# Performance work log

Hardware: AMD Instinct MI355X
Metric: run time of the kernel (lower is better)

## Reference

```python
import jax, jax.numpy as jnp
import numpy as np

B, S, E, H, SN, LMAX = 128, 512, 768, 16, 100, 5
DH = E // H  # 48

def setup_inputs() -> dict:
    key = jax.random.key(0)
    ks = jax.random.split(key, 10)
    idx = jax.random.randint(ks[0], (B, LMAX), 0, S)
    lengths = jax.random.randint(ks[1], (B,), 1, LMAX + 1)
    valid = jnp.arange(LMAX)[None, :] < lengths[:, None]
    locations = jnp.where(valid, idx, -1)
    return {
        "last_hidden_state": jax.random.normal(ks[2], (B, S, E), jnp.float32),
        "sense_emb": jax.random.normal(ks[3], (B, SN, E), jnp.float32),
        "locations": locations,
        "in_proj_weight": jax.random.normal(ks[4], (3 * E, E), jnp.float32) * 0.02,
        "in_proj_bias": jax.random.normal(ks[5], (3 * E,), jnp.float32) * 0.02,
        "out_proj_weight": jax.random.normal(ks[6], (E, E), jnp.float32) * 0.02,
        "out_proj_bias": jax.random.normal(ks[7], (E,), jnp.float32) * 0.02,
        "linear_weight": jax.random.normal(ks[8], (SN, E), jnp.float32) * 0.02,
        "linear_bias": jax.random.normal(ks[9], (SN,), jnp.float32) * 0.02,
    }

def reference(last_hidden_state, sense_emb, locations, in_proj_weight, in_proj_bias,
              out_proj_weight, out_proj_bias, linear_weight, linear_bias):
    # Ragged gather + mean over the valid (non -1) token locations per row.
    mask = (locations != -1)                                   # [B, LMAX]
    safe = jnp.where(mask, locations, 0)                       # [B, LMAX]
    gathered = jnp.take_along_axis(last_hidden_state, safe[..., None], axis=1)  # [B,LMAX,E]
    cnt = mask.sum(axis=1, keepdims=True).astype(last_hidden_state.dtype)
    pun = (gathered * mask[..., None]).sum(axis=1) / cnt       # [B, E]

    # qkv: prepend pun-word embedding to the sense embeddings -> [B, SN+1, E]
    qkv = jnp.concatenate([pun[:, None, :], sense_emb], axis=1)

    # nn.MultiheadAttention with batch_first=False: axis0 = seq (L=B), axis1 = batch (N=SN+1).
    proj = qkv @ in_proj_weight.T + in_proj_bias               # [L, N, 3E]
    q, k, v = jnp.split(proj, 3, axis=-1)
    L, N = qkv.shape[0], qkv.shape[1]
    q = q.reshape(L, N, H, DH) * (DH ** -0.5)
    k = k.reshape(L, N, H, DH)
    v = v.reshape(L, N, H, DH)
    scores = jnp.einsum('lnhd,mnhd->nhlm', q, k)               # [N,H,L,L]
    attn = jax.nn.softmax(scores, axis=-1)
    ctx = jnp.einsum('nhlm,mnhd->lnhd', attn, v).reshape(L, N, E)
    attn_out = ctx @ out_proj_weight.T + out_proj_bias         # [L, N, E]

    res = attn_out[:, 0, :]                                    # [B, E] (batch slot 0)
    res = res @ linear_weight.T + linear_bias                  # [B, SN]
    return res
```

## Files before the change

### kernel.cpp

```cpp
#include <hip/hip_runtime.h>

#define SEQ 512
#define EMB 768
#define K3E 2304
#define DHD 48

__global__ __launch_bounds__(256) void k1_gemm1(
    const float* __restrict__ lhs, const int* __restrict__ loc,
    const float* __restrict__ Bw, const float* __restrict__ bias,
    float* __restrict__ C)
{
  __shared__ float lds[7168];
  const int t  = threadIdx.x;
  const int w  = t >> 6, l = t & 63;
  const int bm = blockIdx.y * 16, bn = blockIdx.x * 32;
  const int tx = l & 7, ty = l >> 3;
  const int gm = l & 15, gq = l >> 4;
  const int bl = l & 31, bh = l >> 5;
  const int kbase = w * 192;
  const int AW = w * 1792, BW = AW + 640;

  int locs[5]; int cnt = 0;
#pragma unroll
  for (int j = 0; j < 5; j++) {
    int v = loc[(bm + gm) * 5 + j];
    locs[j] = v; if (v >= 0) cnt++;
  }
  const float ginv = 1.0f / (float)cnt;
  const float* lrow = lhs + (size_t)(bm + gm) * SEQ * EMB;
  const float* brow = Bw + (size_t)(bn + bl) * EMB;

  float4 aF, bF0, bF1;

#define K1_LOAD(s) {                                                         \
    int k0 = kbase + (s) * 16;                                               \
    float sx=0.f, sy=0.f, sz=0.f, sw=0.f;                                    \
    _Pragma("unroll")                                                        \
    for (int j = 0; j < 5; j++) {                                            \
      int v = locs[j] >= 0 ? locs[j] : 0;                                    \
      float4 wv = *(const float4*)&lrow[(size_t)v * EMB + k0 + gq * 4];      \
      if (locs[j] >= 0) { sx+=wv.x; sy+=wv.y; sz+=wv.z; sw+=wv.w; }          \
    }                                                                        \
    aF = make_float4(sx*ginv, sy*ginv, sz*ginv, sw*ginv);                    \
    bF0 = *(const float4*)&brow[k0 + bh * 8 + 0];                            \
    bF1 = *(const float4*)&brow[k0 + bh * 8 + 4]; }

#define K1_WRITE(b) {                                                        \
    int Ab = AW + (b) * 320;                                                 \
    lds[Ab + (gq*4+0)*20 + gm] = aF.x;                                       \
    lds[Ab + (gq*4+1)*20 + gm] = aF.y;                                       \
    lds[Ab + (gq*4+2)*20 + gm] = aF.z;                                       \
    lds[Ab + (gq*4+3)*20 + gm] = aF.w;                                       \
    int Bb = BW + (b) * 576;                                                 \
    lds[Bb + (bh*8+0)*36 + bl] = bF0.x; lds[Bb + (bh*8+1)*36 + bl] = bF0.y;  \
    lds[Bb + (bh*8+2)*36 + bl] = bF0.z; lds[Bb + (bh*8+3)*36 + bl] = bF0.w;  \
    lds[Bb + (bh*8+4)*36 + bl] = bF1.x; lds[Bb + (bh*8+5)*36 + bl] = bF1.y;  \
    lds[Bb + (bh*8+6)*36 + bl] = bF1.z; lds[Bb + (bh*8+7)*36 + bl] = bF1.w; }

  float acc[2][4] = {};
  K1_LOAD(0); K1_WRITE(0);
  for (int s = 0; s < 12; s++) {
    int b = s & 1;
    if (s < 11) K1_LOAD(s + 1);
    int Ab = AW + b * 320, Bb = BW + b * 576;
#pragma unroll
    for (int kk = 0; kk < 16; kk++) {
      float2 a  = *(float2*)&lds[Ab + kk * 20 + ty * 2];
      float4 bb = *(float4*)&lds[Bb + kk * 36 + tx * 4];
      acc[0][0] += a.x*bb.x; acc[0][1] += a.x*bb.y; acc[0][2] += a.x*bb.z; acc[0][3] += a.x*bb.w;
      acc[1][0] += a.y*bb.x; acc[1][1] += a.y*bb.y; acc[1][2] += a.y*bb.z; acc[1][3] += a.y*bb.w;
    }
    if (s < 11) K1_WRITE(b ^ 1);
  }
#undef K1_LOAD
#undef K1_WRITE

#pragma unroll
  for (int i = 0; i < 2; i++)
    *(float4*)&lds[AW + (ty*2 + i) * 32 + tx * 4] =
        make_float4(acc[i][0], acc[i][1], acc[i][2], acc[i][3]);
  __syncthreads();
  int o = t * 2;
  int m = o >> 5, n = o & 31;
  float2 s0 = *(float2*)&lds[0*1792 + o];
  float2 s1 = *(float2*)&lds[1*1792 + o];
  float2 s2 = *(float2*)&lds[2*1792 + o];
  float2 s3 = *(float2*)&lds[3*1792 + o];
  float2 bb2 = *(const float2*)&bias[bn + n];
  float2 r = make_float2(s0.x+s1.x+s2.x+s3.x+bb2.x, s0.y+s1.y+s2.y+s3.y+bb2.y);
  *(float2*)&C[(size_t)(bm + m) * K3E + bn + n] = r;
}

__global__ __launch_bounds__(256) void k2_attn_wcomb(
    const float* __restrict__ proj, float* __restrict__ ctx,
    const float* __restrict__ wlin, const float* __restrict__ wout,
    float* __restrict__ wcomb)
{
  __shared__ float lds[13312];
  const int t = threadIdx.x;

  if (blockIdx.x < 128) {
    float* ks = lds;
    float* vs = lds + 6656;
    int h  = blockIdx.x >> 3;
    int l0 = (blockIdx.x & 7) * 16;

    for (int i = t; i < 128 * 12; i += 256) {
      int m  = i / 12;
      int dd = (i - m * 12) * 4;
      float4 kv = *(const float4*)&proj[(size_t)m * K3E + EMB     + h * DHD + dd];
      float4 vv = *(const float4*)&proj[(size_t)m * K3E + 2 * EMB + h * DHD + dd];
      *(float4*)&ks[m * 52 + dd] = kv;
      *(float4*)&vs[m * 52 + dd] = vv;
    }

    int l  = t >> 4;
    int g  = t & 15;
    int lg = l0 + l;
    const float scale = 0.14433756729740643f;
    float q[48];
#pragma unroll
    for (int jj = 0; jj < 12; jj++) {
      float4 qv = *(const float4*)&proj[(size_t)lg * K3E + h * DHD + jj * 4];
      q[jj*4+0] = qv.x * scale; q[jj*4+1] = qv.y * scale;
      q[jj*4+2] = qv.z * scale; q[jj*4+3] = qv.w * scale;
    }
    __syncthreads();

    float sv[8];
    float smax = -1e30f;
#pragma unroll
    for (int jm = 0; jm < 8; jm++) {
      int m = g + jm * 16;
      float s = 0.0f;
#pragma unroll
      for (int dq = 0; dq < 12; dq++) {
        float4 kv = *(const float4*)&ks[m * 52 + dq * 4];
        s += q[dq*4+0]*kv.x + q[dq*4+1]*kv.y + q[dq*4+2]*kv.z + q[dq*4+3]*kv.w;
      }
      sv[jm] = s;
      smax = fmaxf(smax, s);
    }
#pragma unroll
    for (int off = 1; off < 16; off <<= 1) smax = fmaxf(smax, __shfl_xor(smax, off));
    float ssum = 0.0f;
#pragma unroll
    for (int jm = 0; jm < 8; jm++) { float e = __expf(sv[jm] - smax); sv[jm] = e; ssum += e; }
#pragma unroll
    for (int off = 1; off < 16; off <<= 1) ssum += __shfl_xor(ssum, off);
    float inv = 1.0f / ssum;
#pragma unroll
    for (int jm = 0; jm < 8; jm++) sv[jm] *= inv;

    float acc[48] = {};
#pragma unroll
    for (int jm = 0; jm < 8; jm++) {
      int m = g + jm * 16;
      float p = sv[jm];
#pragma unroll
      for (int dq = 0; dq < 12; dq++) {
        float4 vv = *(const float4*)&vs[m * 52 + dq * 4];
        acc[dq*4+0] += p*vv.x; acc[dq*4+1] += p*vv.y;
        acc[dq*4+2] += p*vv.z; acc[dq*4+3] += p*vv.w;
      }
    }

    {
      float buf[24];
      if (g & 8) {
#pragma unroll
        for (int d = 0; d < 24; d++) buf[d] = acc[d];
      } else {
#pragma unroll
        for (int d = 0; d < 24; d++) buf[d] = acc[d + 24];
      }
#pragma unroll
      for (int d = 0; d < 24; d++) buf[d] = __shfl_xor(buf[d], 8);
      if (g & 8) {
#pragma unroll
        for (int d = 0; d < 24; d++) acc[d] = acc[d + 24] + buf[d];
      } else {
#pragma unroll
        for (int d = 0; d < 24; d++) acc[d] = acc[d] + buf[d];
      }
    }
    {
      float buf[12];
      if (g & 4) {
#pragma unroll
        for (int d = 0; d < 12; d++) buf[d] = acc[d];
      } else {
#pragma unroll
        for (int d = 0; d < 12; d++) buf[d] = acc[d + 12];
      }
#pragma unroll
      for (int d = 0; d < 12; d++) buf[d] = __shfl_xor(buf[d], 4);
      if (g & 4) {
#pragma unroll
        for (int d = 0; d < 12; d++) acc[d] = acc[d + 12] + buf[d];
      } else {
#pragma unroll
        for (int d = 0; d < 12; d++) acc[d] = acc[d] + buf[d];
      }
    }
    {
      float buf[6];
      if (g & 2) {
#pragma unroll
        for (int d = 0; d < 6; d++) buf[d] = acc[d];
      } else {
#pragma unroll
        for (int d = 0; d < 6; d++) buf[d] = acc[d + 6];
      }
#pragma unroll
      for (int d = 0; d < 6; d++) buf[d] = __shfl_xor(buf[d], 2);
      if (g & 2) {
#pragma unroll
        for (int d = 0; d < 6; d++) acc[d] = acc[d + 6] + buf[d];
      } else {
#pragma unroll
        for (int d = 0; d < 6; d++) acc[d] = acc[d] + buf[d];
      }
    }
    {
      float buf[3];
      if (g & 1) {
#pragma unroll
        for (int d = 0; d < 3; d++) buf[d] = acc[d];
      } else {
#pragma unroll
        for (int d = 0; d < 3; d++) buf[d] = acc[d + 3];
      }
#pragma unroll
      for (int d = 0; d < 3; d++) buf[d] = __shfl_xor(buf[d], 1);
      if (g & 1) {
#pragma unroll
        for (int d = 0; d < 3; d++) acc[d] = acc[d + 3] + buf[d];
      } else {
#pragma unroll
        for (int d = 0; d < 3; d++) acc[d] = acc[d] + buf[d];
      }
    }
#pragma unroll
    for (int j = 0; j < 3; j++) {
      ctx[(size_t)lg * EMB + h * DHD + g * 3 + j] = acc[j];
    }
  } else {
    const int c  = blockIdx.x - 128;
    const int bm = (c / 24) * 16;
    const int bn = (c % 24) * 32;
    const int w  = t >> 6, l = t & 63;
    const int tx = l & 7, ty = l >> 3;
    const int am = l & 15, aq = l >> 4;
    const int wi = l >> 2;
    const int j4 = (l & 3) * 8;
    const int kbase = w * 192;
    const int AW = w * 1792, BW = AW + 640;

    int arow_i = bm + am; if (arow_i > 99) arow_i = 99;
    const float* arow = wlin + (size_t)arow_i * EMB;

    float4 aF, bF0, bF1;

#define W_LOAD(s) {                                                          \
    int k0 = kbase + (s) * 16;                                               \
    aF  = *(const float4*)&arow[k0 + aq * 4];                                \
    const float* wr = wout + (size_t)(k0 + wi) * EMB + bn + j4;              \
    bF0 = *(const float4*)&wr[0];                                            \
    bF1 = *(const float4*)&wr[4]; }

#define W_WRITE(b) {                                                         \
    int Ab = AW + (b) * 320;                                                 \
    lds[Ab + (aq*4+0)*20 + am] = aF.x;                                       \
    lds[Ab + (aq*4+1)*20 + am] = aF.y;                                       \
    lds[Ab + (aq*4+2)*20 + am] = aF.z;                                       \
    lds[Ab + (aq*4+3)*20 + am] = aF.w;                                       \
    int Bb = BW + (b) * 576;                                                 \
    *(float4*)&lds[Bb + wi*36 + j4]     = bF0;                               \
    *(float4*)&lds[Bb + wi*36 + j4 + 4] = bF1; }

    float acc[2][4] = {};
    W_LOAD(0); W_WRITE(0);
    for (int s = 0; s < 12; s++) {
      int b = s & 1;
      if (s < 11) W_LOAD(s + 1);
      int Ab = AW + b * 320, Bb = BW + b * 576;
#pragma unroll
      for (int kk = 0; kk < 16; kk++) {
        float2 a  = *(float2*)&lds[Ab + kk * 20 + ty * 2];
        float4 bb = *(float4*)&lds[Bb + kk * 36 + tx * 4];
        acc[0][0] += a.x*bb.x; acc[0][1] += a.x*bb.y; acc[0][2] += a.x*bb.z; acc[0][3] += a.x*bb.w;
        acc[1][0] += a.y*bb.x; acc[1][1] += a.y*bb.y; acc[1][2] += a.y*bb.z; acc[1][3] += a.y*bb.w;
      }
      if (s < 11) W_WRITE(b ^ 1);
    }
#undef W_LOAD
#undef W_WRITE

#pragma unroll
    for (int i = 0; i < 2; i++)
      *(float4*)&lds[AW + (ty*2 + i) * 32 + tx * 4] =
          make_float4(acc[i][0], acc[i][1], acc[i][2], acc[i][3]);
    __syncthreads();
    int o = t * 2;
    int m = o >> 5, n = o & 31;
    if (bm + m < 100) {
      float2 s0 = *(float2*)&lds[0*1792 + o];
      float2 s1 = *(float2*)&lds[1*1792 + o];
      float2 s2 = *(float2*)&lds[2*1792 + o];
      float2 s3 = *(float2*)&lds[3*1792 + o];
      float2 r = make_float2(s0.x+s1.x+s2.x+s3.x, s0.y+s1.y+s2.y+s3.y);
      *(float2*)&wcomb[(size_t)(bm + m) * EMB + bn + n] = r;
    }
  }
}

__global__ __launch_bounds__(256) void k3_final(
    const float* __restrict__ A, const float* __restrict__ Bw,
    const float* __restrict__ wlin, const float* __restrict__ bout,
    const float* __restrict__ blin, float* __restrict__ C)
{
  __shared__ float lds[7200];
  const int t  = threadIdx.x;
  const int w  = t >> 6, l = t & 63;
  const int bm = blockIdx.y * 16, bn = blockIdx.x * 32;
  const int tx = l & 7, ty = l >> 3;
  const int am = l & 15, aq = l >> 4;
  const int bl = l & 31, bh = l >> 5;
  const int kbase = w * 192;
  const int AW = w * 1792, BW = AW + 640;

  {
    int col = bn + (t >> 3);
    int ks  = (t & 7) * 96;
    float p = 0.f;
    if (col < 100) {
      const float* wr = wlin + (size_t)col * EMB + ks;
#pragma unroll
      for (int j = 0; j < 24; j++) {
        float4 wv = *(const float4*)&wr[j * 4];
        float4 bv = *(const float4*)&bout[ks + j * 4];
        p += wv.x*bv.x + wv.y*bv.y + wv.z*bv.z + wv.w*bv.w;
      }
    }
    p += __shfl_xor(p, 1); p += __shfl_xor(p, 2); p += __shfl_xor(p, 4);
    if ((t & 7) == 0) lds[7168 + (t >> 3)] = p + (col < 100 ? blin[col] : 0.f);
  }

  const float* arow = A + (size_t)(bm + am) * EMB;
  int brow_i = bn + bl; if (brow_i > 99) brow_i = 99;
  const float* brow = Bw + (size_t)brow_i * EMB;

  float4 aF, bF0, bF1;

#define F_LOAD(s) {                                                          \
    int k0 = kbase + (s) * 16;                                               \
    aF  = *(const float4*)&arow[k0 + aq * 4];                                \
    bF0 = *(const float4*)&brow[k0 + bh * 8 + 0];                            \
    bF1 = *(const float4*)&brow[k0 + bh * 8 + 4]; }

#define F_WRITE(b) {                                                         \
    int Ab = AW + (b) * 320;                                                 \
    lds[Ab + (aq*4+0)*20 + am] = aF.x;                                       \
    lds[Ab + (aq*4+1)*20 + am] = aF.y;                                       \
    lds[Ab + (aq*4+2)*20 + am] = aF.z;                                       \
    lds[Ab + (aq*4+3)*20 + am] = aF.w;                                       \
    int Bb = BW + (b) * 576;                                                 \
    lds[Bb + (bh*8+0)*36 + bl] = bF0.x; lds[Bb + (bh*8+1)*36 + bl] = bF0.y;  \
    lds[Bb + (bh*8+2)*36 + bl] = bF0.z; lds[Bb + (bh*8+3)*36 + bl] = bF0.w;  \
    lds[Bb + (bh*8+4)*36 + bl] = bF1.x; lds[Bb + (bh*8+5)*36 + bl] = bF1.y;  \
    lds[Bb + (bh*8+6)*36 + bl] = bF1.z; lds[Bb + (bh*8+7)*36 + bl] = bF1.w; }

  float acc[2][4] = {};
  F_LOAD(0); F_WRITE(0);
  for (int s = 0; s < 12; s++) {
    int b = s & 1;
    if (s < 11) F_LOAD(s + 1);
    int Ab = AW + b * 320, Bb = BW + b * 576;
#pragma unroll
    for (int kk = 0; kk < 16; kk++) {
      float2 a  = *(float2*)&lds[Ab + kk * 20 + ty * 2];
      float4 bb = *(float4*)&lds[Bb + kk * 36 + tx * 4];
      acc[0][0] += a.x*bb.x; acc[0][1] += a.x*bb.y; acc[0][2] += a.x*bb.z; acc[0][3] += a.x*bb.w;
      acc[1][0] += a.y*bb.x; acc[1][1] += a.y*bb.y; acc[1][2] += a.y*bb.z; acc[1][3] += a.y*bb.w;
    }
    if (s < 11) F_WRITE(b ^ 1);
  }
#undef F_LOAD
#undef F_WRITE

#pragma unroll
  for (int i = 0; i < 2; i++)
    *(float4*)&lds[AW + (ty*2 + i) * 32 + tx * 4] =
        make_float4(acc[i][0], acc[i][1], acc[i][2], acc[i][3]);
  __syncthreads();
  int o = t * 2;
  int m = o >> 5, n = o & 31;
#pragma unroll
  for (int j = 0; j < 2; j++) {
    int col = bn + n + j;
    if (col < 100) {
      float v = lds[0*1792 + o + j] + lds[1*1792 + o + j] +
                lds[2*1792 + o + j] + lds[3*1792 + o + j] + lds[7168 + n + j];
      C[(size_t)(bm + m) * 100 + col] = v;
    }
  }
}

extern "C" void kernel_launch(void* const* d_in, const int* in_sizes, int n_in,
                              void* d_out, int out_size, void* d_ws, size_t ws_size,
                              hipStream_t stream) {
  const float* lhs   = (const float*)d_in[0];
  const int*   loc   = (const int*)  d_in[2];
  const float* w_in  = (const float*)d_in[3];
  const float* b_in  = (const float*)d_in[4];
  const float* w_out = (const float*)d_in[5];
  const float* b_out = (const float*)d_in[6];
  const float* w_lin = (const float*)d_in[7];
  const float* b_lin = (const float*)d_in[8];
  float* out = (float*)d_out;

  char* ws = (char*)d_ws;
  float* proj  = (float*)(ws);
  float* ctx   = (float*)(ws + 1179648);
  float* wcomb = (float*)(ws + 1179648 + 393216);

  k1_gemm1<<<dim3(72, 8), 256, 0, stream>>>(lhs, loc, w_in, b_in, proj);
  k2_attn_wcomb<<<296, 256, 0, stream>>>(proj, ctx, w_lin, w_out, wcomb);
  k3_final<<<dim3(4, 8), 256, 0, stream>>>(ctx, wcomb, w_lin, b_out, b_lin, out);
}
```

Baseline: 51.70 us.

## Double split-K waves to 8 per block and hoist pun gathers ahead of GEMM loop

The first projection GEMM and the final GEMM now use 512-thread blocks with 8 waves, each covering 96 of the K dimension instead of 192. Partial sums are reduced across the 8 waves in LDS. In the projection kernel, all the pun-word gather-and-mean loads for a thread's K slice are issued upfront into registers before the GEMM loop, so those scattered loads overlap instead of sitting on the critical path each stage. The changes aim to expose more parallelism and memory-level concurrency, at the cost of more registers, twice the LDS per block, and a larger cross-wave reduction.

```diff
diff --git a/kernel.cpp b/kernel.cpp
--- a/kernel.cpp
+++ b/kernel.cpp
@@ -5,90 +5,102 @@
 #define K3E 2304
 #define DHD 48
 
-__global__ __launch_bounds__(256) void k1_gemm1(
+__global__ __launch_bounds__(512, 4) void k1_proj(
     const float* __restrict__ lhs, const int* __restrict__ loc,
     const float* __restrict__ Bw, const float* __restrict__ bias,
     float* __restrict__ C)
 {
-  __shared__ float lds[7168];
-  const int t  = threadIdx.x;
-  const int w  = t >> 6, l = t & 63;
-  const int bm = blockIdx.y * 16, bn = blockIdx.x * 32;
+  __shared__ float lds[14336];
+  const int t = threadIdx.x;
+  const int w = t >> 6, l = t & 63;
   const int tx = l & 7, ty = l >> 3;
   const int gm = l & 15, gq = l >> 4;
   const int bl = l & 31, bh = l >> 5;
-  const int kbase = w * 192;
+  const int kbase = w * 96;
   const int AW = w * 1792, BW = AW + 640;
-
-  int locs[5]; int cnt = 0;
-#pragma unroll
-  for (int j = 0; j < 5; j++) {
-    int v = loc[(bm + gm) * 5 + j];
-    locs[j] = v; if (v >= 0) cnt++;
-  }
+  const int bm = ((int)blockIdx.x / 72) * 16, bn = ((int)blockIdx.x % 72) * 32;
+
+  int locs[5];
+#pragma unroll
+  for (int j = 0; j < 5; j++) locs[j] = loc[(bm + gm) * 5 + j];
+  int cnt = 0;
+#pragma unroll
+  for (int j = 0; j < 5; j++) if (locs[j] >= 0) cnt++;
   const float ginv = 1.0f / (float)cnt;
   const float* lrow = lhs + (size_t)(bm + gm) * SEQ * EMB;
+
+  float4 pA[6];
+#pragma unroll
+  for (int s = 0; s < 6; s++) {
+    int k0 = kbase + s * 16 + gq * 4;
+    float sx = 0.f, sy = 0.f, sz = 0.f, sw = 0.f;
+#pragma unroll
+    for (int j = 0; j < 5; j++) {
+      int v = locs[j] >= 0 ? locs[j] : 0;
+      float4 wv = *(const float4*)&lrow[(size_t)v * EMB + k0];
+      if (locs[j] >= 0) { sx += wv.x; sy += wv.y; sz += wv.z; sw += wv.w; }
+    }
+    pA[s] = make_float4(sx * ginv, sy * ginv, sz * ginv, sw * ginv);
+  }
+
   const float* brow = Bw + (size_t)(bn + bl) * EMB;
-
-  float4 aF, bF0, bF1;
-
-#define K1_LOAD(s) {                                                         \
+  float4 bF0, bF1;
+  float acc[2][4] = {};
+
+#define B_LOAD(s) {                                                          \
     int k0 = kbase + (s) * 16;                                               \
-    float sx=0.f, sy=0.f, sz=0.f, sw=0.f;                                    \
-    _Pragma("unroll")                                                        \
-    for (int j = 0; j < 5; j++) {                                            \
-      int v = locs[j] >= 0 ? locs[j] : 0;                                    \
-      float4 wv = *(const float4*)&lrow[(size_t)v * EMB + k0 + gq * 4];      \
-      if (locs[j] >= 0) { sx+=wv.x; sy+=wv.y; sz+=wv.z; sw+=wv.w; }          \
-    }                                                                        \
-    aF = make_float4(sx*ginv, sy*ginv, sz*ginv, sw*ginv);                    \
     bF0 = *(const float4*)&brow[k0 + bh * 8 + 0];                            \
     bF1 = *(const float4*)&brow[k0 + bh * 8 + 4]; }
 
-#define K1_WRITE(b) {                                                        \
+#define A_WRITE(b, av) {                                                     \
     int Ab = AW + (b) * 320;                                                 \
-    lds[Ab + (gq*4+0)*20 + gm] = aF.x;                                       \
-    lds[Ab + (gq*4+1)*20 + gm] = aF.y;                                       \
-    lds[Ab + (gq*4+2)*20 + gm] = aF.z;                                       \
-    lds[Ab + (gq*4+3)*20 + gm] = aF.w;                                       \
+    lds[Ab + (gq*4+0)*20 + gm] = (av).x;                                     \
+    lds[Ab + (gq*4+1)*20 + gm] = (av).y;                                     \
+    lds[Ab + (gq*4+2)*20 + gm] = (av).z;                                     \
+    lds[Ab + (gq*4+3)*20 + gm] = (av).w; }
+
+#define B_WRITE(b) {                                                         \
     int Bb = BW + (b) * 576;                                                 \
     lds[Bb + (bh*8+0)*36 + bl] = bF0.x; lds[Bb + (bh*8+1)*36 + bl] = bF0.y;  \
     lds[Bb + (bh*8+2)*36 + bl] = bF0.z; lds[Bb + (bh*8+3)*36 + bl] = bF0.w;  \
     lds[Bb + (bh*8+4)*36 + bl] = bF1.x; lds[Bb + (bh*8+5)*36 + bl] = bF1.y;  \
     lds[Bb + (bh*8+6)*36 + bl] = bF1.z; lds[Bb + (bh*8+7)*36 + bl] = bF1.w; }
 
-  float acc[2][4] = {};
-  K1_LOAD(0); K1_WRITE(0);
-  for (int s = 0; s < 12; s++) {
+#define INNER(b) {                                                           \
+    int Ab = AW + (b) * 320, Bb = BW + (b) * 576;                            \
+    _Pragma("unroll")                                                        \
+    for (int kk = 0; kk < 16; kk++) {                                        \
+      float2 a  = *(float2*)&lds[Ab + kk * 20 + ty * 2];                     \
+      float4 bb = *(float4*)&lds[Bb + kk * 36 + tx * 4];                     \
+      acc[0][0] += a.x*bb.x; acc[0][1] += a.x*bb.y;                          \
+      acc[0][2] += a.x*bb.z; acc[0][3] += a.x*bb.w;                          \
+      acc[1][0] += a.y*bb.x; acc[1][1] += a.y*bb.y;                          \
+      acc[1][2] += a.y*bb.z; acc[1][3] += a.y*bb.w;                          \
+    } }
+
+  B_LOAD(0); A_WRITE(0, pA[0]); B_WRITE(0);
+#pragma unroll
+  for (int s = 0; s < 6; s++) {
     int b = s & 1;
-    if (s < 11) K1_LOAD(s + 1);
-    int Ab = AW + b * 320, Bb = BW + b * 576;
-#pragma unroll
-    for (int kk = 0; kk < 16; kk++) {
-      float2 a  = *(float2*)&lds[Ab + kk * 20 + ty * 2];
-      float4 bb = *(float4*)&lds[Bb + kk * 36 + tx * 4];
-      acc[0][0] += a.x*bb.x; acc[0][1] += a.x*bb.y; acc[0][2] += a.x*bb.z; acc[0][3] += a.x*bb.w;
-      acc[1][0] += a.y*bb.x; acc[1][1] += a.y*bb.y; acc[1][2] += a.y*bb.z; acc[1][3] += a.y*bb.w;
-    }
-    if (s < 11) K1_WRITE(b ^ 1);
-  }
-#undef K1_LOAD
-#undef K1_WRITE
+    if (s < 5) B_LOAD(s + 1);
+    INNER(b);
+    if (s < 5) { A_WRITE(b ^ 1, pA[s + 1]); B_WRITE(b ^ 1); }
+  }
+#undef B_LOAD
+#undef A_WRITE
+#undef B_WRITE
+#undef INNER
 
 #pragma unroll
   for (int i = 0; i < 2; i++)
     *(float4*)&lds[AW + (ty*2 + i) * 32 + tx * 4] =
         make_float4(acc[i][0], acc[i][1], acc[i][2], acc[i][3]);
   __syncthreads();
-  int o = t * 2;
-  int m = o >> 5, n = o & 31;
-  float2 s0 = *(float2*)&lds[0*1792 + o];
-  float2 s1 = *(float2*)&lds[1*1792 + o];
-  float2 s2 = *(float2*)&lds[2*1792 + o];
-  float2 s3 = *(float2*)&lds[3*1792 + o];
-  float2 bb2 = *(const float2*)&bias[bn + n];
-  float2 r = make_float2(s0.x+s1.x+s2.x+s3.x+bb2.x, s0.y+s1.y+s2.y+s3.y+bb2.y);
-  *(float2*)&C[(size_t)(bm + m) * K3E + bn + n] = r;
+  int m = t >> 5, n = t & 31;
+  float v = lds[0*1792 + t] + lds[1*1792 + t] + lds[2*1792 + t] + lds[3*1792 + t]
+          + lds[4*1792 + t] + lds[5*1792 + t] + lds[6*1792 + t] + lds[7*1792 + t]
+          + bias[bn + n];
+  C[(size_t)(bm + m) * K3E + bn + n] = v;
 }
 
 __global__ __launch_bounds__(256) void k2_attn_wcomb(
@@ -247,8 +259,7 @@
     }
   } else {
     const int c  = blockIdx.x - 128;
-    const int bm = (c / 24) * 16;
-    const int bn = (c % 24) * 32;
+    const int bm = (c / 24) * 16, bn = (c % 24) * 32;
     const int w  = t >> 6, l = t & 63;
     const int tx = l & 7, ty = l >> 3;
     const int am = l & 15, aq = l >> 4;
@@ -315,22 +326,22 @@
   }
 }
 
-__global__ __launch_bounds__(256) void k3_final(
+__global__ __launch_bounds__(512, 4) void k3_final(
     const float* __restrict__ A, const float* __restrict__ Bw,
     const float* __restrict__ wlin, const float* __restrict__ bout,
     const float* __restrict__ blin, float* __restrict__ C)
 {
-  __shared__ float lds[7200];
-  const int t  = threadIdx.x;
-  const int w  = t >> 6, l = t & 63;
+  __shared__ float lds[14368];
+  const int t = threadIdx.x;
+  const int w = t >> 6, l = t & 63;
   const int bm = blockIdx.y * 16, bn = blockIdx.x * 32;
   const int tx = l & 7, ty = l >> 3;
-  const int am = l & 15, aq = l >> 4;
+  const int gm = l & 15, gq = l >> 4;
   const int bl = l & 31, bh = l >> 5;
-  const int kbase = w * 192;
+  const int kbase = w * 96;
   const int AW = w * 1792, BW = AW + 640;
 
-  {
+  if (t < 256) {
     int col = bn + (t >> 3);
     int ks  = (t & 7) * 96;
     float p = 0.f;
@@ -344,10 +355,10 @@
       }
     }
     p += __shfl_xor(p, 1); p += __shfl_xor(p, 2); p += __shfl_xor(p, 4);
-    if ((t & 7) == 0) lds[7168 + (t >> 3)] = p + (col < 100 ? blin[col] : 0.f);
-  }
-
-  const float* arow = A + (size_t)(bm + am) * EMB;
+    if ((t & 7) == 0) lds[14336 + (t >> 3)] = p + (col < 100 ? blin[col] : 0.f);
+  }
+
+  const float* arow = A + (size_t)(bm + gm) * EMB;
   int brow_i = bn + bl; if (brow_i > 99) brow_i = 99;
   const float* brow = Bw + (size_t)brow_i * EMB;
 
@@ -355,16 +366,16 @@
 
 #define F_LOAD(s) {                                                          \
     int k0 = kbase + (s) * 16;                                               \
-    aF  = *(const float4*)&arow[k0 + aq * 4];                                \
+    aF  = *(const float4*)&arow[k0 + gq * 4];                                \
     bF0 = *(const float4*)&brow[k0 + bh * 8 + 0];                            \
     bF1 = *(const float4*)&brow[k0 + bh * 8 + 4]; }
 
 #define F_WRITE(b) {                                                         \
     int Ab = AW + (b) * 320;                                                 \
-    lds[Ab + (aq*4+0)*20 + am] = aF.x;                                       \
-    lds[Ab + (aq*4+1)*20 + am] = aF.y;                                       \
-    lds[Ab + (aq*4+2)*20 + am] = aF.z;                                       \
-    lds[Ab + (aq*4+3)*20 + am] = aF.w;                                       \
+    lds[Ab + (gq*4+0)*20 + gm] = aF.x;                                       \
+    lds[Ab + (gq*4+1)*20 + gm] = aF.y;                                       \
+    lds[Ab + (gq*4+2)*20 + gm] = aF.z;                                       \
+    lds[Ab + (gq*4+3)*20 + gm] = aF.w;                                       \
     int Bb = BW + (b) * 576;                                                 \
     lds[Bb + (bh*8+0)*36 + bl] = bF0.x; lds[Bb + (bh*8+1)*36 + bl] = bF0.y;  \
     lds[Bb + (bh*8+2)*36 + bl] = bF0.z; lds[Bb + (bh*8+3)*36 + bl] = bF0.w;  \
@@ -373,9 +384,9 @@
 
   float acc[2][4] = {};
   F_LOAD(0); F_WRITE(0);
-  for (int s = 0; s < 12; s++) {
+  for (int s = 0; s < 6; s++) {
     int b = s & 1;
-    if (s < 11) F_LOAD(s + 1);
+    if (s < 5) F_LOAD(s + 1);
     int Ab = AW + b * 320, Bb = BW + b * 576;
 #pragma unroll
     for (int kk = 0; kk < 16; kk++) {
@@ -384,7 +395,7 @@
       acc[0][0] += a.x*bb.x; acc[0][1] += a.x*bb.y; acc[0][2] += a.x*bb.z; acc[0][3] += a.x*bb.w;
       acc[1][0] += a.y*bb.x; acc[1][1] += a.y*bb.y; acc[1][2] += a.y*bb.z; acc[1][3] += a.y*bb.w;
     }
-    if (s < 11) F_WRITE(b ^ 1);
+    if (s < 5) F_WRITE(b ^ 1);
   }
 #undef F_LOAD
 #undef F_WRITE
@@ -394,16 +405,13 @@
     *(float4*)&lds[AW + (ty*2 + i) * 32 + tx * 4] =
         make_float4(acc[i][0], acc[i][1], acc[i][2], acc[i][3]);
   __syncthreads();
-  int o = t * 2;
-  int m = o >> 5, n = o & 31;
-#pragma unroll
-  for (int j = 0; j < 2; j++) {
-    int col = bn + n + j;
-    if (col < 100) {
-      float v = lds[0*1792 + o + j] + lds[1*1792 + o + j] +
-                lds[2*1792 + o + j] + lds[3*1792 + o + j] + lds[7168 + n + j];
-      C[(size_t)(bm + m) * 100 + col] = v;
-    }
+  int m = t >> 5, n = t & 31;
+  int col = bn + n;
+  if (col < 100) {
+    float v = lds[0*1792 + t] + lds[1*1792 + t] + lds[2*1792 + t] + lds[3*1792 + t]
+            + lds[4*1792 + t] + lds[5*1792 + t] + lds[6*1792 + t] + lds[7*1792 + t]
+            + lds[14336 + n];
+    C[(size_t)(bm + m) * 100 + col] = v;
   }
 }
 
@@ -423,9 +431,9 @@
   char* ws = (char*)d_ws;
   float* proj  = (float*)(ws);
   float* ctx   = (float*)(ws + 1179648);
-  float* wcomb = (float*)(ws + 1179648 + 393216);
-
-  k1_gemm1<<<dim3(72, 8), 256, 0, stream>>>(lhs, loc, w_in, b_in, proj);
+  float* wcomb = (float*)(ws + 1572864);
+
+  k1_proj<<<576, 512, 0, stream>>>(lhs, loc, w_in, b_in, proj);
   k2_attn_wcomb<<<296, 256, 0, stream>>>(proj, ctx, w_lin, w_out, wcomb);
-  k3_final<<<dim3(4, 8), 256, 0, stream>>>(ctx, wcomb, w_lin, b_out, b_lin, out);
+  k3_final<<<dim3(4, 8), 512, 0, stream>>>(ctx, wcomb, w_lin, b_out, b_lin, out);
 }
```

Measured after the change: 61.23 us. +18.4%, slower.
